# Optimization experiments

Measured on AMD Instinct MI355X. Metric: run time of the kernel, lower is better.

## Reference

```python
import jax, jax.numpy as jnp
import numpy as np

# Model dims
B, N, D_MODEL, N_HEADS = 8, 4096, 512, 8
EXPAND = 2
D1 = (EXPAND * D_MODEL) // N_HEADS * N_HEADS      # 1024
HEAD_DIM = D1 // N_HEADS                          # 128
RANK, NK = 32, 16
GAMMA = 0.999


def setup_inputs() -> dict:
    key = jax.random.key(0)
    ks = jax.random.split(key, 24)

    def p(i, shape, std=0.02):
        return std * jax.random.normal(ks[i], shape, dtype=jnp.float32)

    def toep_params(i0):
        # SKI low-rank Toeplitz operator params: kernel values at NK inducing
        # lag positions, factorized as (h, nk, r) @ (h, r, d), plus lag-0 term.
        return (p(i0, (N_HEADS, 1, HEAD_DIM), 1.0),        # zero lag
                p(i0 + 1, (N_HEADS, NK, RANK), 0.1),       # pos lags A
                p(i0 + 2, (N_HEADS, RANK, HEAD_DIM), 0.1), # pos lags B
                p(i0 + 3, (N_HEADS, NK, RANK), 0.1),       # neg lags A
                p(i0 + 4, (N_HEADS, RANK, HEAD_DIM), 0.1)) # neg lags B

    t1 = toep_params(7)
    t2 = toep_params(12)
    return {
        'x': jax.random.normal(ks[0], (B, N, D_MODEL), dtype=jnp.float32),
        'u_w': p(1, (D1, D_MODEL)), 'u_b': p(2, (D1,)),
        'v_w': p(3, (D1, D_MODEL)), 'v_b': p(4, (D1,)),
        'o_w': p(5, (D_MODEL, D1)), 'o_b': p(6, (D_MODEL,)),
        't1_zero': t1[0], 't1_pa': t1[1], 't1_pb': t1[2], 't1_na': t1[3], 't1_nb': t1[4],
        't2_zero': t2[0], 't2_pa': t2[1], 't2_pb': t2[2], 't2_na': t2[3], 't2_nb': t2[4],
    }


def _build_kernel(zero, pos_a, pos_b, neg_a, neg_b, n):
    """Build circular-conv kernel a of shape (h, 2n, d): a[k]=t(k), a[2n-k]=t(-k)."""
    h, nk, _ = pos_a.shape
    d = pos_b.shape[-1]
    tm_pos = jnp.einsum('hkr,hrd->hkd', pos_a, pos_b)   # kernel at inducing lags
    tm_neg = jnp.einsum('hkr,hrd->hkd', neg_a, neg_b)
    lags = jnp.arange(1, n, dtype=jnp.float32)          # lags 1..n-1
    # linear interpolation from NK inducing points to n-1 lags
    pos_f = (lags - 1.0) / max(n - 2, 1) * (nk - 1)
    lo = jnp.floor(pos_f).astype(jnp.int32)
    hi = jnp.minimum(lo + 1, nk - 1)
    w = (pos_f - lo)[None, :, None]
    decay = (GAMMA ** lags)[None, :, None]              # exponential decay bias
    t_pos = ((1.0 - w) * tm_pos[:, lo] + w * tm_pos[:, hi]) * decay
    t_neg = ((1.0 - w) * tm_neg[:, lo] + w * tm_neg[:, hi]) * decay
    return jnp.concatenate(
        [zero, t_pos, jnp.zeros((h, 1, d), t_pos.dtype), jnp.flip(t_neg, axis=1)],
        axis=1)


def _toep_apply(x, zero, pos_a, pos_b, neg_a, neg_b):
    # x: (b, n, g) with g = h*d; multi-head Toeplitz mixing along axis 1 via FFT.
    b, n, g = x.shape
    h = zero.shape[0]
    d = g // h
    xh = x.reshape(b, n, h, d).transpose(0, 2, 1, 3)    # (b, h, n, d)
    a = _build_kernel(zero, pos_a, pos_b, neg_a, neg_b, n)  # (h, 2n, d)
    y = jnp.fft.irfft(
        jnp.fft.rfft(xh, 2 * n, axis=2) * jnp.fft.rfft(a, axis=1)[None],
        2 * n, axis=2)[:, :, :n]
    return y.transpose(0, 2, 1, 3).reshape(b, n, g)


def reference(x, u_w, u_b, v_w, v_b, o_w, o_b,
              t1_zero, t1_pa, t1_pb, t1_na, t1_nb,
              t2_zero, t2_pa, t2_pb, t2_na, t2_nb):
    b, n, _ = x.shape
    H = int(np.sqrt(n))
    W = n // H
    u = jax.nn.silu(x @ u_w.T + u_b)
    v = jax.nn.silu(x @ v_w.T + v_b)
    g = v.shape[-1]
    t1 = (t1_zero, t1_pa, t1_pb, t1_na, t1_nb)
    t2 = (t2_zero, t2_pa, t2_pb, t2_na, t2_nb)
    # path 1: mix along W (rows) with toep1, then along H (cols) with toep2
    o1 = _toep_apply(v.reshape(b * H, W, g), *t1)
    o1 = o1.reshape(b, H, W, g).transpose(0, 2, 1, 3).reshape(b * W, H, g)
    o1 = _toep_apply(o1, *t2)
    o1 = o1.reshape(b, W, H, g).transpose(0, 2, 1, 3).reshape(b, H * W, g)
    # path 2: mix along H with toep2, then along W with toep1
    v2 = v.reshape(b, H, W, g).transpose(0, 2, 1, 3).reshape(b * W, H, g)
    o2 = _toep_apply(v2, *t2)
    o2 = o2.reshape(b, W, H, g).transpose(0, 2, 1, 3).reshape(b * H, W, g)
    o2 = _toep_apply(o2, *t1)
    o2 = o2.reshape(b, H * W, g)
    # SiLU gate + output projection
    return (u * (o1 + o2)) @ o_w.T + o_b
```

## Files before the change

### kernel.cpp

```cpp
#include <hip/hip_runtime.h>
#include <hip/hip_bf16.h>
#include <hip/hip_fp16.h>

typedef __bf16 bf16;
typedef bf16 bf16x2 __attribute__((ext_vector_type(2)));
typedef bf16 bf16x4 __attribute__((ext_vector_type(4)));
typedef bf16 bf16x8 __attribute__((ext_vector_type(8)));
typedef float f32x2 __attribute__((ext_vector_type(2)));
typedef float f32x4 __attribute__((ext_vector_type(4)));

__device__ __forceinline__ void gload_lds16(const void* g, void* l) {
  __builtin_amdgcn_global_load_lds((__attribute__((address_space(1))) void*)g,
                                   (__attribute__((address_space(3))) void*)l,
                                   16, 0, 0);
}

__device__ __forceinline__ f32x2 fma2(f32x2 a, f32x2 b, f32x2 c) {
  return __builtin_elementwise_fma(a, b, c);
}


__global__ void cast_f32_to_bf16(const float* __restrict__ in, bf16* __restrict__ out, int n4) {
  int i = blockIdx.x * blockDim.x + threadIdx.x;
  if (i >= n4) return;
  float4 v = ((const float4*)in)[i];
  bf16x4 o = {(bf16)v.x, (bf16)v.y, (bf16)v.z, (bf16)v.w};
  ((bf16x4*)out)[i] = o;
}

__global__ void cast_w3(const float* __restrict__ uw, const float* __restrict__ vw,
                        const float* __restrict__ ow,
                        bf16* __restrict__ wuv, bf16* __restrict__ owb) {
  int t = blockIdx.x * 256 + threadIdx.x;
  int r = t >> 17;
  int i = t & 131071;
  const float* src = (r == 0) ? uw : (r == 1) ? vw : ow;
  bf16* dst = (r == 2) ? owb : (wuv + (r == 1) * 524288);
  float4 v = ((const float4*)src)[i];
  bf16x4 o = {(bf16)v.x, (bf16)v.y, (bf16)v.z, (bf16)v.w};
  ((bf16x4*)dst)[i] = o;
}

__global__ void concat_bias(const float* __restrict__ ub, const float* __restrict__ vb,
                            float* __restrict__ buv) {
  int i = blockIdx.x * blockDim.x + threadIdx.x;
  if (i < 1024) { buv[i] = ub[i]; buv[1024 + i] = vb[i]; }
}

__global__ void build_tkf(const float* __restrict__ zero, const float* __restrict__ pa,
                          const float* __restrict__ pb, const float* __restrict__ na,
                          const float* __restrict__ nb, float* __restrict__ Tkf,
                          float scale) {
  int idx = blockIdx.x * blockDim.x + threadIdx.x;
  if (idx >= 8 * 127 * 128) return;
  int d = idx & 127;
  int lagIdx = (idx >> 7) % 127;
  int h = idx / (128 * 127);
  int lag = lagIdx - 63;
  float val;
  if (lag == 0) {
    val = zero[h * 128 + d];
  } else {
    int k = lag > 0 ? lag : -lag;
    const float* A  = lag > 0 ? pa : na;
    const float* Bm = lag > 0 ? pb : nb;
    float pos_f = (float)(k - 1) * (15.0f / 62.0f);
    int lo = (int)floorf(pos_f);
    int hi = min(lo + 1, 15);
    float w = pos_f - (float)lo;
    float s = 0.f;
    for (int r = 0; r < 32; ++r) {
      float c = (1.f - w) * A[(h * 16 + lo) * 32 + r] + w * A[(h * 16 + hi) * 32 + r];
      s += c * Bm[(h * 32 + r) * 128 + d];
    }
    val = s * powf(0.999f, (float)k);
  }
  Tkf[idx] = val * scale;
}


template<int MODE>
__global__ __launch_bounds__(256)
void gemm_bt(const bf16* __restrict__ A, const bf16* __restrict__ B,
             const float* __restrict__ bias,
             bf16* __restrict__ out_u, bf16* __restrict__ out_v,
             float* __restrict__ out_f,
             int M, int N, int K) {
  __shared__ bf16 As[128 * 32];
  __shared__ bf16 Bs[128 * 32];
  const int tid  = threadIdx.x;
  const int lane = tid & 63;
  const int nbn  = N >> 7;
  const int cpx  = gridDim.x >> 3;
  const int swz  = (blockIdx.x & 7) * cpx + (blockIdx.x >> 3);
  const int br   = (swz / nbn) << 7;
  const int bc   = (swz % nbn) << 7;
  const int wub  = __builtin_amdgcn_readfirstlane(tid & 192);

  f32x4 acc[4][4] = {};

  auto stage = [&](int k0) {
#pragma unroll
    for (int r = 0; r < 2; ++r) {
      const int flat = r * 256 + tid;
      const int row  = flat >> 2;
      const int kc   = (flat & 3) << 3;
      gload_lds16(A + ((size_t)(br + row) * K + k0 + kc),
                  (char*)As + (size_t)(r * 256 + wub) * 16);
      gload_lds16(B + ((size_t)(bc + row) * K + k0 + kc),
                  (char*)Bs + (size_t)(r * 256 + wub) * 16);
    }
  };

  const int l15 = lane & 15;
  const int lk  = (lane >> 4) << 3;
  const int wr  = ((tid >> 7) & 1) << 6;
  const int wc  = ((tid >> 6) & 1) << 6;

  auto compute = [&]() {
    bf16x8 af[4], bfr[4];
#pragma unroll
    for (int m = 0; m < 4; ++m)
      af[m] = *(const bf16x8*)&As[(wr + m * 16 + l15) * 32 + lk];
#pragma unroll
    for (int n = 0; n < 4; ++n)
      bfr[n] = *(const bf16x8*)&Bs[(wc + n * 16 + l15) * 32 + lk];
#pragma unroll
    for (int m = 0; m < 4; ++m)
#pragma unroll
      for (int n = 0; n < 4; ++n)
        acc[m][n] = __builtin_amdgcn_mfma_f32_16x16x32_bf16(af[m], bfr[n], acc[m][n], 0, 0, 0);
  };

  stage(0);
  __syncthreads();
  for (int k0 = 32; k0 < K; k0 += 32) {
    compute();
    __syncthreads();
    stage(k0);
    __syncthreads();
  }
  compute();

  const int lr4 = (lane >> 4) << 2;
  if (MODE == 0) {
    const bool isU = (bc < 1024);
    bf16* outp = isU ? out_u : out_v;
#pragma unroll
    for (int m = 0; m < 4; ++m) {
#pragma unroll
      for (int n = 0; n < 4; ++n) {
        const int col  = bc + wc + n * 16 + l15;
        const int ocol = (bc & 1023) + wc + n * 16 + l15;
        const float bv = bias[col];
#pragma unroll
        for (int r = 0; r < 4; ++r) {
          const int row = br + wr + m * 16 + lr4 + r;
          float xv = acc[m][n][r] + bv;
          float s  = xv / (1.f + __expf(-xv));
          outp[(size_t)row * 1024 + ocol] = (bf16)s;
        }
      }
    }
  } else {
#pragma unroll
    for (int m = 0; m < 4; ++m) {
#pragma unroll
      for (int n = 0; n < 4; ++n) {
        const int col  = bc + wc + n * 16 + l15;
        const float bv = bias[col];
#pragma unroll
        for (int r = 0; r < 4; ++r) {
          const int row = br + wr + m * 16 + lr4 + r;
          out_f[(size_t)row * N + col] = acc[m][n][r] + bv;
        }
      }
    }
  }
}


#define VROW 130

template<int FUSE>
__global__ __launch_bounds__(256, 3)
void toep_pass(const bf16* __restrict__ in, const float* __restrict__ Tkf,
               const bf16* __restrict__ ufuse, bf16* __restrict__ out,
               int stride_j, int stride_row) {
  __shared__ float vbuf[64 * VROW];
  const int tid    = threadIdx.x;
  const int lane   = tid & 63;
  const int rowIdx = blockIdx.x >> 3;
  const int head   = blockIdx.x & 7;
  const size_t base = (size_t)(rowIdx >> 6) * 4194304
                    + (size_t)(rowIdx & 63) * stride_row + head * 128;

  const int i0 = (tid >> 6) << 4;
  const float* tg = Tkf + head * 127 * 128 + (lane << 1);

  f32x2 t[31];
#pragma unroll
  for (int s = 0; s < 31; ++s)
    t[s] = *(const f32x2*)(tg + (i0 + 48 + s) * 128);

#pragma unroll
  for (int it = 0; it < 2; ++it) {
    int c  = it * 256 + tid;
    int j  = c >> 3;
    int cg = c & 7;
    const bf16* p = in + base + (size_t)j * stride_j + cg * 16;
    bf16x8 a0 = *(const bf16x8*)p;
    bf16x8 a1 = *(const bf16x8*)(p + 8);
    f32x4 f0 = {(float)a0[0], (float)a0[1], (float)a0[2], (float)a0[3]};
    f32x4 f1 = {(float)a0[4], (float)a0[5], (float)a0[6], (float)a0[7]};
    f32x4 f2 = {(float)a1[0], (float)a1[1], (float)a1[2], (float)a1[3]};
    f32x4 f3 = {(float)a1[4], (float)a1[5], (float)a1[6], (float)a1[7]};
    float* dst = &vbuf[j * VROW + cg * 16];
    *(f32x4*)(dst)      = f0;
    *(f32x4*)(dst + 4)  = f1;
    *(f32x4*)(dst + 8)  = f2;
    *(f32x4*)(dst + 12) = f3;
  }
  __syncthreads();

  f32x2 acc[16] = {};
#pragma unroll
  for (int jb = 0; jb < 4; ++jb) {
    f32x2 p16[16];
    if (jb < 3) {
#pragma unroll
      for (int s = 0; s < 16; ++s)
        p16[s] = *(const f32x2*)(tg + (i0 - 16 * (jb + 1) + 48 + s) * 128);
    }
#pragma unroll
    for (int jj = 0; jj < 16; ++jj) {
      f32x2 v2 = *(const f32x2*)&vbuf[(jb * 16 + jj) * VROW + (lane << 1)];
#pragma unroll
      for (int ii = 0; ii < 16; ++ii)
        acc[ii] = fma2(t[ii - jj + 15], v2, acc[ii]);
    }
    if (jb < 3) {
#pragma unroll
      for (int s = 30; s >= 16; --s) t[s] = t[s - 16];
#pragma unroll
      for (int s = 0; s < 16; ++s) t[s] = p16[s];
    }
  }

  const int d0 = lane << 1;
#pragma unroll
  for (int ii = 0; ii < 16; ++ii) {
    const size_t oidx = base + (size_t)(i0 + ii) * stride_j + d0;
    float a0 = acc[ii].x, a1 = acc[ii].y;
    if (FUSE) {
      bf16x2 uu = *(const bf16x2*)(ufuse + oidx);
      a0 *= (float)uu[0];
      a1 *= (float)uu[1];
    }
    bf16x2 o2 = {(bf16)a0, (bf16)a1};
    *(bf16x2*)(out + oidx) = o2;
  }
}


extern "C" void kernel_launch(void* const* d_in, const int* in_sizes, int n_in,
                              void* d_out, int out_size, void* d_ws, size_t ws_size,
                              hipStream_t stream) {
  const float* x    = (const float*)d_in[0];
  const float* u_w  = (const float*)d_in[1];
  const float* u_b  = (const float*)d_in[2];
  const float* v_w  = (const float*)d_in[3];
  const float* v_b  = (const float*)d_in[4];
  const float* o_w  = (const float*)d_in[5];
  const float* o_b  = (const float*)d_in[6];
  const float* t1z  = (const float*)d_in[7];
  const float* t1pa = (const float*)d_in[8];
  const float* t1pb = (const float*)d_in[9];
  const float* t1na = (const float*)d_in[10];
  const float* t1nb = (const float*)d_in[11];
  const float* t2z  = (const float*)d_in[12];
  const float* t2pa = (const float*)d_in[13];
  const float* t2pb = (const float*)d_in[14];
  const float* t2na = (const float*)d_in[15];
  const float* t2nb = (const float*)d_in[16];

  char* ws = (char*)d_ws;
  size_t off = 0;
  auto alloc = [&](size_t bytes) {
    char* p = ws + off;
    off += (bytes + 255) & ~(size_t)255;
    return p;
  };
  bf16*  xb   = (bf16*)alloc(32768ull * 512 * 2);
  bf16*  wuv  = (bf16*)alloc(2048ull * 512 * 2);
  bf16*  owb  = (bf16*)alloc(512ull * 1024 * 2);
  float* buv  = (float*)alloc(2048ull * 4);
  float* Tkf1 = (float*)alloc(8ull * 127 * 128 * 4);
  float* Tkf2 = (float*)alloc(8ull * 127 * 128 * 4);
  bf16*  u    = (bf16*)alloc(32768ull * 1024 * 2);
  bf16*  v    = (bf16*)alloc(32768ull * 1024 * 2);
  bf16*  tmid = (bf16*)alloc(32768ull * 1024 * 2);
  bf16*  g    = v;

  cast_f32_to_bf16<<<16384, 256, 0, stream>>>(x, xb, 16777216 / 4);
  cast_w3<<<1536, 256, 0, stream>>>(u_w, v_w, o_w, wuv, owb);
  concat_bias<<<4, 256, 0, stream>>>(u_b, v_b, buv);
  build_tkf<<<508, 256, 0, stream>>>(t1z, t1pa, t1pb, t1na, t1nb, Tkf1, 1.0f);
  build_tkf<<<508, 256, 0, stream>>>(t2z, t2pa, t2pb, t2na, t2nb, Tkf2, 2.0f);

  gemm_bt<0><<<4096, 256, 0, stream>>>(xb, wuv, buv, u, v, nullptr, 32768, 2048, 512);
  toep_pass<0><<<4096, 256, 0, stream>>>(v, Tkf1, nullptr, tmid, 1024, 65536);
  toep_pass<1><<<4096, 256, 0, stream>>>(tmid, Tkf2, u, g, 65536, 1024);
  gemm_bt<1><<<1024, 256, 0, stream>>>(g, owb, o_b, nullptr, nullptr, (float*)d_out,
                                       32768, 512, 1024);
}
```

Before: 318.0 us.

## Replace 128x128 GEMM with 256x256 double-buffered swizzled-LDS MFMA kernel

Both projection GEMMs now use a new kernel with 512 threads per block and 256x256 output tiles. It has a K-step of 64 and double-buffered LDS (128KB) loaded with direct global-to-LDS copies. An XOR swizzle on the LDS layout avoids bank conflicts, and s_setprio plus intra-iteration barriers interleave the MFMA phases. The goal is more data reuse per byte loaded and overlap of next-tile loads with compute. The cost is fewer, larger blocks and only one block per CU because of LDS size, which leaves the second GEMM with just 256 blocks.

```diff
diff --git a/kernel.cpp b/kernel.cpp
--- a/kernel.cpp
+++ b/kernel.cpp
@@ -80,82 +80,98 @@
 
 
 template<int MODE>
-__global__ __launch_bounds__(256)
-void gemm_bt(const bf16* __restrict__ A, const bf16* __restrict__ B,
-             const float* __restrict__ bias,
-             bf16* __restrict__ out_u, bf16* __restrict__ out_v,
-             float* __restrict__ out_f,
-             int M, int N, int K) {
-  __shared__ bf16 As[128 * 32];
-  __shared__ bf16 Bs[128 * 32];
+__global__ __launch_bounds__(512, 2)
+void gemm8(const bf16* __restrict__ A, const bf16* __restrict__ Bm,
+           const float* __restrict__ bias,
+           bf16* __restrict__ out_u, bf16* __restrict__ out_v,
+           float* __restrict__ out_f, int M, int N, int K) {
+  __shared__ __align__(16) char lds[131072];
   const int tid  = threadIdx.x;
   const int lane = tid & 63;
-  const int nbn  = N >> 7;
+  const int l15  = lane & 15;
+  const int lk16 = ((lane >> 4) & 3) << 4;
+  const int w    = tid >> 6;
+  const int wm   = (w >> 2) << 7;
+  const int wn   = (w & 3) << 6;
+  const int nbn  = N >> 8;
   const int cpx  = gridDim.x >> 3;
-  const int swz  = (blockIdx.x & 7) * cpx + (blockIdx.x >> 3);
-  const int br   = (swz / nbn) << 7;
-  const int bc   = (swz % nbn) << 7;
-  const int wub  = __builtin_amdgcn_readfirstlane(tid & 192);
-
-  f32x4 acc[4][4] = {};
-
-  auto stage = [&](int k0) {
-#pragma unroll
-    for (int r = 0; r < 2; ++r) {
-      const int flat = r * 256 + tid;
-      const int row  = flat >> 2;
-      const int kc   = (flat & 3) << 3;
-      gload_lds16(A + ((size_t)(br + row) * K + k0 + kc),
-                  (char*)As + (size_t)(r * 256 + wub) * 16);
-      gload_lds16(B + ((size_t)(bc + row) * K + k0 + kc),
-                  (char*)Bs + (size_t)(r * 256 + wub) * 16);
+  const int swzb = (blockIdx.x & 7) * cpx + (blockIdx.x >> 3);
+  const int br   = (swzb / nbn) << 8;
+  const int bc   = (swzb % nbn) << 8;
+  const int wub  = __builtin_amdgcn_readfirstlane(tid & 448);
+  const int nkt  = K >> 6;
+
+  f32x4 acc[8][4] = {};
+
+  auto stage = [&](int kt, int b) {
+    const int k0 = kt << 6;
+    char* Al = lds + b * 65536;
+    char* Bl = Al + 32768;
+#pragma unroll
+    for (int g = 0; g < 4; ++g) {
+      const int flat = g * 512 + tid;
+      const int row  = flat >> 3;
+      const int cb   = ((flat & 7) << 4) ^ ((row & 7) << 4);
+      gload_lds16((const char*)(A  + (size_t)(br + row) * K + k0) + cb,
+                  Al + (g * 512 + wub) * 16);
+      gload_lds16((const char*)(Bm + (size_t)(bc + row) * K + k0) + cb,
+                  Bl + (g * 512 + wub) * 16);
     }
   };
 
-  const int l15 = lane & 15;
-  const int lk  = (lane >> 4) << 3;
-  const int wr  = ((tid >> 7) & 1) << 6;
-  const int wc  = ((tid >> 6) & 1) << 6;
-
-  auto compute = [&]() {
-    bf16x8 af[4], bfr[4];
-#pragma unroll
-    for (int m = 0; m < 4; ++m)
-      af[m] = *(const bf16x8*)&As[(wr + m * 16 + l15) * 32 + lk];
-#pragma unroll
-    for (int n = 0; n < 4; ++n)
-      bfr[n] = *(const bf16x8*)&Bs[(wc + n * 16 + l15) * 32 + lk];
-#pragma unroll
-    for (int m = 0; m < 4; ++m)
-#pragma unroll
-      for (int n = 0; n < 4; ++n)
-        acc[m][n] = __builtin_amdgcn_mfma_f32_16x16x32_bf16(af[m], bfr[n], acc[m][n], 0, 0, 0);
-  };
-
-  stage(0);
+  stage(0, 0);
   __syncthreads();
-  for (int k0 = 32; k0 < K; k0 += 32) {
-    compute();
+
+  for (int kt = 0; kt < nkt; ++kt) {
+    const int b = kt & 1;
+    const char* Ab = lds + b * 65536;
+    const char* Bb = Ab + 32768;
+    if (kt + 1 < nkt) stage(kt + 1, b ^ 1);
+#pragma unroll
+    for (int ks = 0; ks < 2; ++ks) {
+      bf16x8 bfr[4];
+#pragma unroll
+      for (int n = 0; n < 4; ++n) {
+        const int row = wn + n * 16 + l15;
+        bfr[n] = *(const bf16x8*)(Bb + row * 128 + (((ks << 6) | lk16) ^ ((row & 7) << 4)));
+      }
+#pragma unroll
+      for (int ph = 0; ph < 2; ++ph) {
+        bf16x8 af[4];
+#pragma unroll
+        for (int mi = 0; mi < 4; ++mi) {
+          const int row = wm + (ph * 4 + mi) * 16 + l15;
+          af[mi] = *(const bf16x8*)(Ab + row * 128 + (((ks << 6) | lk16) ^ ((row & 7) << 4)));
+        }
+        __builtin_amdgcn_s_setprio(1);
+#pragma unroll
+        for (int mi = 0; mi < 4; ++mi)
+#pragma unroll
+          for (int n = 0; n < 4; ++n)
+            acc[ph * 4 + mi][n] = __builtin_amdgcn_mfma_f32_16x16x32_bf16(
+                af[mi], bfr[n], acc[ph * 4 + mi][n], 0, 0, 0);
+        __builtin_amdgcn_s_setprio(0);
+        if (ks * 2 + ph < 3) __builtin_amdgcn_s_barrier();
+      }
+    }
     __syncthreads();
-    stage(k0);
-    __syncthreads();
-  }
-  compute();
-
-  const int lr4 = (lane >> 4) << 2;
+  }
+
+  const int lr4 = ((lane >> 4) & 3) << 2;
   if (MODE == 0) {
     const bool isU = (bc < 1024);
     bf16* outp = isU ? out_u : out_v;
-#pragma unroll
-    for (int m = 0; m < 4; ++m) {
+    const int obc = bc & 1023;
+#pragma unroll
+    for (int m = 0; m < 8; ++m) {
 #pragma unroll
       for (int n = 0; n < 4; ++n) {
-        const int col  = bc + wc + n * 16 + l15;
-        const int ocol = (bc & 1023) + wc + n * 16 + l15;
-        const float bv = bias[col];
+        const int colg = bc + wn + n * 16 + l15;
+        const int ocol = obc + wn + n * 16 + l15;
+        const float bv = bias[colg];
 #pragma unroll
         for (int r = 0; r < 4; ++r) {
-          const int row = br + wr + m * 16 + lr4 + r;
+          const int row = br + wm + m * 16 + lr4 + r;
           float xv = acc[m][n][r] + bv;
           float s  = xv / (1.f + __expf(-xv));
           outp[(size_t)row * 1024 + ocol] = (bf16)s;
@@ -164,14 +180,14 @@
     }
   } else {
 #pragma unroll
-    for (int m = 0; m < 4; ++m) {
+    for (int m = 0; m < 8; ++m) {
 #pragma unroll
       for (int n = 0; n < 4; ++n) {
-        const int col  = bc + wc + n * 16 + l15;
+        const int col = bc + wn + n * 16 + l15;
         const float bv = bias[col];
 #pragma unroll
         for (int r = 0; r < 4; ++r) {
-          const int row = br + wr + m * 16 + lr4 + r;
+          const int row = br + wm + m * 16 + lr4 + r;
           out_f[(size_t)row * N + col] = acc[m][n][r] + bv;
         }
       }
@@ -308,9 +324,9 @@
   build_tkf<<<508, 256, 0, stream>>>(t1z, t1pa, t1pb, t1na, t1nb, Tkf1, 1.0f);
   build_tkf<<<508, 256, 0, stream>>>(t2z, t2pa, t2pb, t2na, t2nb, Tkf2, 2.0f);
 
-  gemm_bt<0><<<4096, 256, 0, stream>>>(xb, wuv, buv, u, v, nullptr, 32768, 2048, 512);
+  gemm8<0><<<1024, 512, 0, stream>>>(xb, wuv, buv, u, v, nullptr, 32768, 2048, 512);
   toep_pass<0><<<4096, 256, 0, stream>>>(v, Tkf1, nullptr, tmid, 1024, 65536);
   toep_pass<1><<<4096, 256, 0, stream>>>(tmid, Tkf2, u, g, 65536, 1024);
-  gemm_bt<1><<<1024, 256, 0, stream>>>(g, owb, o_b, nullptr, nullptr, (float*)d_out,
-                                       32768, 512, 1024);
-}
+  gemm8<1><<<256, 512, 0, stream>>>(g, owb, o_b, nullptr, nullptr, (float*)d_out,
+                                    32768, 512, 1024);
+}
```

Measured after the change: 303.3 us. -4.6%, faster.
